# Optimization experiments

Measured on AMD Instinct MI355X. Metric: run time of the kernel, lower is better.

Reference implementation:

```python
import jax, jax.numpy as jnp
import numpy as np

BATCH, MAXPV = 32, 50
RULENUM, PROPNUM = 256, 256  # must be equal (eye(rulenum) * property_importance)
ENT_DIM, RULE_DIM = 128, 128
ENTITYNUM = 50000
THRESHOLD = 0.5


def _l2norm(x, eps=1e-12):
    # F.normalize(p=2, dim=-1)
    n = jnp.linalg.norm(x, axis=-1, keepdims=True)
    return x / jnp.clip(n, eps)


def setup_inputs() -> dict:
    key = jax.random.key(0)
    ks = jax.random.split(key, 20)
    d_in = ENT_DIM + RULE_DIM
    inp = {
        'property': jax.random.randint(ks[0], (BATCH, MAXPV), 0, ENTITYNUM),
        'value': jax.random.randint(ks[1], (BATCH, MAXPV), 0, ENTITYNUM),
        'samemask': jax.random.randint(ks[2], (BATCH, MAXPV), 0, 2),
        'padmask': jax.random.randint(ks[3], (BATCH, MAXPV), 0, 2),
        'rule_embedding': jax.random.normal(ks[4], (RULENUM, RULE_DIM), jnp.float32),
        'entity_table': jax.random.normal(ks[5], (ENTITYNUM, ENT_DIM), jnp.float32),
        # Linear weights stored (in, out); concat order in the original is (p_emb, rule_emb)
        'fc1_w': jax.random.normal(ks[6], (d_in, ENT_DIM), jnp.float32),
        'fc1_b': jax.random.normal(ks[7], (ENT_DIM,), jnp.float32) * 0.02,
        'fc2_w': jax.random.normal(ks[8], (d_in, ENT_DIM), jnp.float32),
        'fc2_b': jax.random.normal(ks[9], (ENT_DIM,), jnp.float32) * 0.02,
        'fc3_w': jax.random.normal(ks[10], (d_in, ENT_DIM), jnp.float32),
        'fc3_b': jax.random.normal(ks[11], (ENT_DIM,), jnp.float32) * 0.02,
        'fc4_w': jax.random.normal(ks[12], (ENT_DIM, 1), jnp.float32) * 0.05,
        'fc4_b': jax.random.normal(ks[13], (1,), jnp.float32) * 0.02,
        'fc5_w': jax.random.normal(ks[14], (ENT_DIM, 1), jnp.float32) * 0.05,
        'fc5_b': jax.random.normal(ks[15], (1,), jnp.float32) * 0.02,
        'fc6_w': jax.random.normal(ks[16], (ENT_DIM, ENT_DIM), jnp.float32) * 0.05,
        'fc6_b': jax.random.normal(ks[17], (ENT_DIM,), jnp.float32) * 0.02,
    }
    return inp


def reference(property, value, samemask, padmask, rule_embedding, entity_table,
              fc1_w, fc1_b, fc2_w, fc2_b, fc3_w, fc3_b,
              fc4_w, fc4_b, fc5_w, fc5_b, fc6_w, fc6_b):
    E = entity_table.shape[1]
    R = rule_embedding.shape[0]
    P = R  # propertynum == rulenum (required by eye() regularizer)

    p_emb = _l2norm(entity_table[property])   # (B, M, E)
    v_emb = _l2norm(entity_table[value])      # (B, M, E)
    r_emb = _l2norm(rule_embedding)           # (R, Dr)

    # cat(p, rule) -> Linear decomposed into two smaller matmuls (same math)
    def branch(w, b):
        return p_emb @ w[:E], r_emb @ w[E:] + b  # (B,M,Eo), (R,Eo)

    # s1 branch
    pa, ra = branch(fc1_w, fc1_b)
    h1 = jax.nn.relu(pa[:, None, :, :] + ra[None, :, None, :])   # (B,R,M,E)
    s1 = jax.nn.sigmoid(h1 @ fc4_w + fc4_b)[..., 0]              # (B,R,M)

    # p branch
    pb, rb = branch(fc2_w, fc2_b)
    h2 = jax.nn.relu(pb[:, None, :, :] + rb[None, :, None, :])
    p = jax.nn.sigmoid(h2 @ fc5_w + fc5_b)[..., 0]               # (B,R,M)

    # s2 branch
    pc, rc = branch(fc3_w, fc3_b)
    h3 = jax.nn.relu(pc[:, None, :, :] + rc[None, :, None, :])
    gv = _l2norm(h3 @ fc6_w + fc6_b)                             # (B,R,M,E)
    vb = v_emb[:, None, :, :]                                    # (B,1,M,E)
    denom = jnp.clip(jnp.linalg.norm(vb, axis=-1) * jnp.linalg.norm(gv, axis=-1), 1e-8)
    cos = jnp.sum(vb * gv, axis=-1) / denom
    s2 = 0.5 * cos + 0.5                                         # (B,R,M)

    score = p + (1.0 - p) * s2
    score = jnp.where(samemask[:, None, :] == 1, s1 * score, 1.0 - s1)

    # property importance K: fc1/fc4 on cat(prop_emb, rule_emb)
    prop_emb = _l2norm(entity_table[:P])                         # propertyids = arange(P)
    pi_h = jax.nn.relu((prop_emb @ fc1_w[:E])[None, :, :]
                       + (r_emb @ fc1_w[E:] + fc1_b)[:, None, :])  # (R,P,E)
    pi = jax.nn.sigmoid(pi_h @ fc4_w + fc4_b)[..., 0]            # (R,P)

    rule_mask = jnp.sum(pi * (pi > THRESHOLD), axis=-1) + 1.0    # (R,)

    score = score * padmask[:, None, :].astype(score.dtype)
    score = score * (s1 > THRESHOLD)
    score = jnp.sum(score, axis=-1) / rule_mask[None, :]          # (B,R)
    pooledscore = jnp.max(score, axis=1)                          # (B,)

    diag = jnp.eye(R, dtype=pi.dtype)
    reg = pi * diag + (1.0 - pi) * (1.0 - diag)
    reg = -jnp.log(reg + 1e-8) * (1.0 - diag + diag * R)
    reg_logits = jnp.mean(reg)
    return pooledscore, reg_logits
```

## Files before the change

kernel.cpp:

```cpp
#include <hip/hip_runtime.h>
#include <hip/hip_bf16.h>

#define BATCH 32
#define MAXPV 50
#define RN 256
#define PN 256
#define DIM 128
#define NI (BATCH*MAXPV)

typedef unsigned short u16;
typedef __attribute__((ext_vector_type(8))) short short8;
typedef __attribute__((ext_vector_type(4))) float f32x4;

#define F4C(v,c) ((c)==0?(v).x:(c)==1?(v).y:(c)==2?(v).z:(v).w)

__device__ float g_pa[NI*DIM], g_pb[NI*DIM], g_pc[NI*DIM];
__device__ float g_pp1[PN*DIM];
__device__ __attribute__((aligned(16))) float g_ra[RN*DIM];
__device__ __attribute__((aligned(16))) float g_rb[RN*DIM];
__device__ float g_rmask[RN], g_regp[RN];
__device__ float g_scores[(size_t)NI*RN];
__device__ short8 g_bfrag[8][4][64];
__device__ __attribute__((aligned(16))) float g_rcA[16*4*64*8];

__device__ __forceinline__ float bf2f(u16 u){ return __uint_as_float(((unsigned)u)<<16); }
__device__ __forceinline__ float LD(const void* p, size_t i, bool bf){
    return bf ? bf2f(((const u16*)p)[i]) : ((const float*)p)[i];
}
__device__ __forceinline__ int LDI(const void* p, size_t i, bool w64){
    return w64 ? (int)((const long long*)p)[i] : ((const int*)p)[i];
}
__device__ __forceinline__ short f2bf(float f){
    unsigned u = __float_as_uint(f);
    u = (u + 0x7FFFu + ((u>>16)&1u)) >> 16;
    return (short)u;
}
__device__ __forceinline__ unsigned f2bf2(float x, float y){
    float2 f; f.x=x; f.y=y;
    __hip_bfloat162 h = __float22bfloat162_rn(f);
    union { __hip_bfloat162 h; unsigned u; } c; c.h=h; return c.u;
}
__device__ __forceinline__ bool det_bf16(const void* ent){
    int l = threadIdx.x & 63;
    u16 v = ((const u16*)ent)[(size_t)2*(l*4)*977];
    int e = (v>>7)&0xFF;
    return __popcll(__ballot(e>=120 && e<=133)) >= 48;
}
__device__ __forceinline__ bool det_i64(const void* prop){
    int l = threadIdx.x & 63;
    bool z = (l<32) ? (((const unsigned*)prop)[2*l+1]==0u) : false;
    return __popcll(__ballot(z)) >= 30;
}
__device__ __forceinline__ float wred(float v){
#pragma unroll
    for(int o=32;o;o>>=1) v += __shfl_xor(v,o,64);
    return v;
}
__device__ __forceinline__ double wredd(double v){
#pragma unroll
    for(int o=32;o;o>>=1) v += __shfl_xor(v,o,64);
    return v;
}
__device__ __forceinline__ float wmax(float v){
#pragma unroll
    for(int o=32;o;o>>=1) v = fmaxf(v,__shfl_xor(v,o,64));
    return v;
}

__global__ __launch_bounds__(256) void k_pre(
    const void* __restrict__ ent, const void* __restrict__ rule,
    const void* __restrict__ prop, const void* __restrict__ fc6w,
    const void* __restrict__ fc1w, const void* __restrict__ fc2w, const void* __restrict__ fc3w,
    const void* __restrict__ fc1b, const void* __restrict__ fc2b, const void* __restrict__ fc3b){
    const bool bf = det_bf16(ent);
    const int blk = blockIdx.x, tid = threadIdx.x;
    if(blk >= 364){
        int nt = blk-364;
        int ks = tid>>6, lane = tid&63;
        int n = nt*16 + (lane&15);
        int k0 = ks*32 + (lane>>4)*8;
        short8 v;
#pragma unroll
        for(int j=0;j<8;j++) v[j] = f2bf(LD(fc6w,(size_t)(k0+j)*DIM + n, bf));
        g_bfrag[nt][ks][lane] = v;
        if(nt==0){ g_rmask[tid] = 1.f; g_regp[tid] = 0.f; }
        return;
    }
    __shared__ float s_w[64*DIM];
    __shared__ float s_in[16*DIM];
    __shared__ float s_bias[DIM];
    const void* w; size_t woff=0; const void* bptr=nullptr;
    float* out=nullptr; int row0; int mode=0; int srcsel;
    if(blk < 300){
        int wsel = blk/100; row0 = (blk%100)*16; srcsel = 0;
        w   = (wsel==0)?fc1w:(wsel==1)?fc2w:fc3w;
        out = (wsel==0)?g_pa:(wsel==1)?g_pb:g_pc;
    } else if(blk < 348){
        int rblk = blk-300; int wsel = rblk>>4; row0 = (rblk&15)*16; srcsel = 1;
        w    = (wsel==0)?fc1w:(wsel==1)?fc2w:fc3w;
        bptr = (wsel==0)?fc1b:(wsel==1)?fc2b:fc3b;
        woff = DIM*DIM; mode = wsel+1;
    } else { row0=(blk-348)*16; w=fc1w; out=g_pp1; srcsel=2; }
    const bool w64 = (srcsel==0) ? det_i64(prop) : false;
    {
        const int l = tid & 63;
        for(int it=0; it<4; it++){
            int lr = it*4 + (tid>>6);
            int row = row0 + lr;
            const void* src; size_t off;
            if(srcsel==0){ src=ent;  off=(size_t)LDI(prop,row,w64)*DIM; }
            else if(srcsel==1){ src=rule; off=(size_t)row*DIM; }
            else { src=ent; off=(size_t)row*DIM; }
            float a = LD(src,off+l,bf), b = LD(src,off+l+64,bf);
            float n = fmaxf(sqrtf((float)wredd((double)a*a+(double)b*b)), 1e-12f);
            s_in[lr*DIM+l]=a/n; s_in[lr*DIM+l+64]=b/n;
        }
    }
    if(tid<DIM) s_bias[tid] = bptr ? LD(bptr,tid,bf) : 0.f;
    const int j = tid & 127;
    const int rb8 = (tid>>7)*8;
    double acc[8] = {0,0,0,0,0,0,0,0};
    for(int half=0; half<2; half++){
        __syncthreads();
        for(int t=tid; t<64*DIM; t+=256)
            s_w[t] = LD(w, woff + (size_t)(half*64 + (t>>7))*DIM + (t&127), bf);
        __syncthreads();
        for(int k=0;k<64;k++){
            float wk = s_w[k*DIM + j];
#pragma unroll
            for(int rr=0;rr<8;rr++)
                acc[rr] += (double)s_in[(rb8+rr)*DIM + half*64 + k]*(double)wk;
        }
    }
    const double bj = (double)s_bias[j];
#pragma unroll
    for(int rr=0;rr<8;rr++){
        const int row = row0 + rb8 + rr;
        const float vv = (float)(bj + acc[rr]);
        if(mode==0)      out[(size_t)row*DIM + j] = vv;
        else if(mode==1) g_ra[(size_t)row*DIM + j] = vv;
        else if(mode==2) g_rb[(size_t)row*DIM + j] = vv;
        else {
            int mt=row>>4, am=row&15, ks=j>>5, quad=(j>>3)&3, jj=j&7;
            g_rcA[((mt*4+ks)*64 + quad*16+am)*8 + jj] = vv;
        }
    }
}

__global__ __launch_bounds__(256) void k_score(
    const void* __restrict__ ent, const void* __restrict__ prop, const void* __restrict__ val,
    const void* __restrict__ same, const void* __restrict__ pad,
    const void* __restrict__ fc4w, const void* __restrict__ fc4b,
    const void* __restrict__ fc5w, const void* __restrict__ fc5b,
    const void* __restrict__ fc6b){
    const int blk = blockIdx.x, tid = threadIdx.x;
    if(blk < 64){
        const bool bf = det_bf16(ent);
        __shared__ float s_a[4][DIM];
        __shared__ double s_pf4[DIM];
        const int i0 = blk*4;
        if(tid<DIM) s_pf4[tid]=(double)LD(fc4w,tid,bf);
        for(int t=tid; t<4*DIM; t+=256){
            int ii=t>>7, k=t&127;
            s_a[ii][k] = g_pp1[(size_t)(i0+ii)*DIM+k];
        }
        __syncthreads();
        const int r = tid;
        const float4* rap = (const float4*)&g_ra[(size_t)r*DIM];
        double d0=0.0, d1=0.0, d2=0.0, d3=0.0;
#pragma unroll 4
        for(int x=0; x<32; x++){
            const float4 ra = rap[x];
#pragma unroll
            for(int cc=0; cc<4; cc++){
                const int k = x*4 + cc;
                const float rav = F4C(ra,cc);
                const double f4k = s_pf4[k];
                d0 += (double)fmaxf(s_a[0][k]+rav,0.f)*f4k;
                d1 += (double)fmaxf(s_a[1][k]+rav,0.f)*f4k;
                d2 += (double)fmaxf(s_a[2][k]+rav,0.f)*f4k;
                d3 += (double)fmaxf(s_a[3][k]+rav,0.f)*f4k;
            }
        }
        const double b4 = (double)LD(fc4b,0,bf);
        double d[4] = {d0,d1,d2,d3};
        float mask_sum = 0.f, reg_sum = 0.f;
#pragma unroll
        for(int ii=0;ii<4;ii++){
            int p = i0 + ii;
            double sd = d[ii] + b4;
            float piv = 1.f/(1.f+expf(-(float)sd));
            if(sd > 0.0) mask_sum += piv;
            float eff = (p==r) ? piv : (1.f - piv);
            float wgt = (p==r) ? (float)RN : 1.f;
            reg_sum += -logf(eff + 1e-8f)*wgt;
        }
        atomicAdd(&g_rmask[r], mask_sum);
        atomicAdd(&g_regp[r], reg_sum);
        return;
    }
    const int ib = blk - 64;
    const int i = ib >> 1, h = ib & 1;
    const bool w64 = det_i64(prop);
    if(LDI(pad,i,w64)!=1) return;
    const bool issame = (LDI(same,i,w64)==1);
    const bool bf = det_bf16(ent);

    __shared__ float s_pa[DIM], s_pb[DIM], s_pc[DIM], s_v[DIM], s_f5[DIM];
    __shared__ double s_f4[DIM];
    __shared__ float s_s1[128], s_p[128];
    __shared__ float s_st[128][4][2];

    if(tid < DIM){
        s_pa[tid] = g_pa[(size_t)i*DIM + tid];
        s_pb[tid] = g_pb[(size_t)i*DIM + tid];
        s_pc[tid] = g_pc[(size_t)i*DIM + tid];
        s_f4[tid] = (double)LD(fc4w,tid,bf);
        s_f5[tid] = LD(fc5w,tid,bf);
    } else if(tid < 192){
        const int l = tid - 128;
        size_t off = (size_t)LDI(val,i,w64)*DIM;
        float a = LD(ent,off+l,bf), b = LD(ent,off+l+64,bf);
        float n = fmaxf(sqrtf((float)wredd((double)a*a+(double)b*b)), 1e-12f);
        s_v[l]=a/n; s_v[l+64]=b/n;
    }
    __syncthreads();

    const int rr = tid & 127;
    const int r = h*128 + rr;
    if(tid < 128){
        const float4* rap = (const float4*)&g_ra[(size_t)r*DIM];
        double d = 0.0;
#pragma unroll 4
        for(int x=0; x<32; x++){
            const float4 ra = rap[x];
            d += (double)fmaxf(s_pa[x*4+0]+ra.x,0.f)*s_f4[x*4+0];
            d += (double)fmaxf(s_pa[x*4+1]+ra.y,0.f)*s_f4[x*4+1];
            d += (double)fmaxf(s_pa[x*4+2]+ra.z,0.f)*s_f4[x*4+2];
            d += (double)fmaxf(s_pa[x*4+3]+ra.w,0.f)*s_f4[x*4+3];
        }
        const double b4 = (double)LD(fc4b,0,bf);
        double sd = d + b4;
        float s1v = 1.f/(1.f+expf(-(float)sd));
        if(issame) s_s1[rr] = (sd > 0.0) ? s1v : -s1v;
        else g_scores[(size_t)i*RN + r] = (sd > 0.0) ? (1.f - s1v) : 0.f;
    } else if(issame){
        const float4* rbp = (const float4*)&g_rb[(size_t)r*DIM];
        float pq = 0.f;
#pragma unroll 4
        for(int x=0; x<32; x++){
            const float4 rb = rbp[x];
            pq = fmaf(fmaxf(s_pb[x*4+0]+rb.x,0.f), s_f5[x*4+0], pq);
            pq = fmaf(fmaxf(s_pb[x*4+1]+rb.y,0.f), s_f5[x*4+1], pq);
            pq = fmaf(fmaxf(s_pb[x*4+2]+rb.z,0.f), s_f5[x*4+2], pq);
            pq = fmaf(fmaxf(s_pb[x*4+3]+rb.w,0.f), s_f5[x*4+3], pq);
        }
        const float b5 = LD(fc5b,0,bf);
        s_p[rr] = 1.f/(1.f+expf(-(pq + b5)));
    }
    if(!issame) return;
    __syncthreads();

    const int w = tid>>6, l = tid&63;
    const int am = l&15, quad = l>>4;
    short8 bA[4], bB[4];
#pragma unroll
    for(int ks=0; ks<4; ks++){ bA[ks]=g_bfrag[2*w][ks][l]; bB[ks]=g_bfrag[2*w+1][ks][l]; }
    const int n0 = w*32 + am, n1 = n0 + 16;
    const float v0 = s_v[n0], v1 = s_v[n1];
    const float b60 = LD(fc6b, n0, bf), b61 = LD(fc6b, n1, bf);
    float vl = s_v[l], vh = s_v[l+64];
    const float nvb = sqrtf(wred(vl*vl + vh*vh));

    int mt = h*8;
    float4 c[8];
#pragma unroll
    for(int ks=0; ks<4; ks++){
        const float* rp = &g_rcA[((mt*4+ks)*64 + l)*8];
        c[2*ks]   = *(const float4*)rp;
        c[2*ks+1] = *(const float4*)(rp+4);
    }
    for(int mtl=0; mtl<8; mtl++){
        float4 n[8];
        if(mtl < 7){
#pragma unroll
            for(int ks=0; ks<4; ks++){
                const float* rp = &g_rcA[(((mt+1)*4+ks)*64 + l)*8];
                n[2*ks]   = *(const float4*)rp;
                n[2*ks+1] = *(const float4*)(rp+4);
            }
        }
        short8 a[4];
#pragma unroll
        for(int ks=0; ks<4; ks++){
            const float4 p0 = *(const float4*)&s_pc[ks*32 + quad*8];
            const float4 p1 = *(const float4*)&s_pc[ks*32 + quad*8 + 4];
            const float4 c0 = c[2*ks], c1 = c[2*ks+1];
            union { short8 s; unsigned u[4]; } t;
            t.u[0] = f2bf2(fmaxf(p0.x+c0.x,0.f), fmaxf(p0.y+c0.y,0.f));
            t.u[1] = f2bf2(fmaxf(p0.z+c0.z,0.f), fmaxf(p0.w+c0.w,0.f));
            t.u[2] = f2bf2(fmaxf(p1.x+c1.x,0.f), fmaxf(p1.y+c1.y,0.f));
            t.u[3] = f2bf2(fmaxf(p1.z+c1.z,0.f), fmaxf(p1.w+c1.w,0.f));
            a[ks] = t.s;
        }
        f32x4 acc0 = {0.f,0.f,0.f,0.f}, acc1 = {0.f,0.f,0.f,0.f};
#pragma unroll
        for(int ks=0; ks<4; ks++){
            acc0 = __builtin_amdgcn_mfma_f32_16x16x32_bf16(a[ks], bA[ks], acc0, 0,0,0);
            acc1 = __builtin_amdgcn_mfma_f32_16x16x32_bf16(a[ks], bB[ks], acc1, 0,0,0);
        }
#pragma unroll
        for(int q=0; q<4; q++){
            float x0 = acc0[q] + b60;
            float x1 = acc1[q] + b61;
            float ss = x0*x0 + x1*x1;
            float dv = x0*v0 + x1*v1;
#pragma unroll
            for(int o=1;o<16;o<<=1){ ss += __shfl_xor(ss,o,64); dv += __shfl_xor(dv,o,64); }
            if(am==0){
                int row = mtl*16 + quad*4 + q;
                s_st[row][w][0] = ss;
                s_st[row][w][1] = dv;
            }
        }
#pragma unroll
        for(int x=0;x<8;x++) c[x] = n[x];
        mt++;
    }
    __syncthreads();
    if(tid < 128){
        const int r2 = h*128 + tid;
        float ss = s_st[tid][0][0]+s_st[tid][1][0]+s_st[tid][2][0]+s_st[tid][3][0];
        float dv = s_st[tid][0][1]+s_st[tid][1][1]+s_st[tid][2][1]+s_st[tid][3][1];
        float s1 = fabsf(s_s1[tid]);
        float gate = (s_s1[tid] > 0.f) ? 1.f : 0.f;
        float pp = s_p[tid];
        float nx = sqrtf(ss);
        float clipnx = fmaxf(nx, 1e-12f);
        float gvn = nx/clipnx;
        float denom = fmaxf(nvb*gvn, 1e-8f);
        float cosv = (dv/clipnx)/denom;
        float s2 = 0.5f*cosv + 0.5f;
        float sc = s1*(pp + (1.f-pp)*s2);
        g_scores[(size_t)i*RN + r2] = sc * gate;
    }
}

__global__ void k_fin(float* __restrict__ out, const void* __restrict__ prop,
                      const void* __restrict__ same, const void* __restrict__ pad){
    const bool w64 = det_i64(prop);
    const int blk = blockIdx.x, tid = threadIdx.x;
    const int w = tid>>6, l = tid&63;
    __shared__ float s[4];
    if(blk < 32){
        __shared__ int s_pad[MAXPV];
        if(tid < MAXPV) s_pad[tid] = LDI(pad, (size_t)blk*MAXPV + tid, w64);
        __syncthreads();
        float ssum = 0.f;
        for(int pv=0; pv<MAXPV; pv++){
            if(!s_pad[pv]) continue;
            ssum += g_scores[((size_t)blk*MAXPV + pv)*RN + tid];
        }
        float sc = ssum / g_rmask[tid];
        float m = wmax(sc);
        if(l==0) s[w]=m;
        __syncthreads();
        if(tid==0) out[blk] = fmaxf(fmaxf(s[0],s[1]), fmaxf(s[2],s[3]));
    } else {
        float v = g_regp[tid];
        v = wred(v);
        if(l==0) s[w]=v;
        __syncthreads();
        if(tid==0) out[32] = (s[0]+s[1]+s[2]+s[3]) / (float)(RN*PN);
    }
}

extern "C" void kernel_launch(void* const* d_in, const int* in_sizes, int n_in,
                              void* d_out, int out_size, void* d_ws, size_t ws_size,
                              hipStream_t stream){
    int map[18]; for(int i=0;i<18;i++) map[i]=i;
    if(n_in>=18 && in_sizes[0]==6400000){
        const int a[18] = {14,17,16,13,15,0,2,1,4,3,6,5,8,7,10,9,12,11};
        for(int i=0;i<18;i++) map[i]=a[i];
    }
    const void* prop = d_in[map[0]];
    const void* val  = d_in[map[1]];
    const void* same = d_in[map[2]];
    const void* pad  = d_in[map[3]];
    const void* rule = d_in[map[4]];
    const void* ent  = d_in[map[5]];
    const void* fc1w = d_in[map[6]];
    const void* fc1b = d_in[map[7]];
    const void* fc2w = d_in[map[8]];
    const void* fc2b = d_in[map[9]];
    const void* fc3w = d_in[map[10]];
    const void* fc3b = d_in[map[11]];
    const void* fc4w = d_in[map[12]];
    const void* fc4b = d_in[map[13]];
    const void* fc5w = d_in[map[14]];
    const void* fc5b = d_in[map[15]];
    const void* fc6w = d_in[map[16]];
    const void* fc6b = d_in[map[17]];

    k_pre<<<372, 256, 0, stream>>>(ent, rule, prop, fc6w,
                                   fc1w, fc2w, fc3w, fc1b, fc2b, fc3b);
    k_score<<<NI*2+64, 256, 0, stream>>>(ent, prop, val, same, pad,
                                         fc4w, fc4b, fc5w, fc5b, fc6b);
    k_fin<<<33, 256, 0, stream>>>((float*)d_out, prop, same, pad);
}
```

Measured before the change: 212.1 us.

## Compact active items into same/diff worklists to skip padded blocks

k_pre gains extra blocks that scan pad and same masks and use atomic counters to build two compacted worklists in workspace: same items paired with their value index, and non-same items. k_score then maps blocks onto these lists, so blocks for padded items exit immediately and non-same items run a lighter specialised path without the fc5/fc6 and MFMA work. Format flags are computed once and stored, and launch bounds now request higher occupancy. This adds a memset, atomics and an extra indirection, and about half of the launched blocks now exit early.

```diff
diff --git a/kernel.cpp b/kernel.cpp
--- a/kernel.cpp
+++ b/kernel.cpp
@@ -11,8 +11,6 @@
 typedef unsigned short u16;
 typedef __attribute__((ext_vector_type(8))) short short8;
 typedef __attribute__((ext_vector_type(4))) float f32x4;
-
-#define F4C(v,c) ((c)==0?(v).x:(c)==1?(v).y:(c)==2?(v).z:(v).w)
 
 __device__ float g_pa[NI*DIM], g_pb[NI*DIM], g_pc[NI*DIM];
 __device__ float g_pp1[PN*DIM];
@@ -23,6 +21,9 @@
 __device__ short8 g_bfrag[8][4][64];
 __device__ __attribute__((aligned(16))) float g_rcA[16*4*64*8];
 
+#define WS_WLS(ws)  ((int2*)((ws)+4))
+#define WS_WLD(ws)  ((ws)+4+3200)
+
 __device__ __forceinline__ float bf2f(u16 u){ return __uint_as_float(((unsigned)u)<<16); }
 __device__ __forceinline__ float LD(const void* p, size_t i, bool bf){
     return bf ? bf2f(((const u16*)p)[i]) : ((const float*)p)[i];
@@ -69,11 +70,32 @@
 
 __global__ __launch_bounds__(256) void k_pre(
     const void* __restrict__ ent, const void* __restrict__ rule,
-    const void* __restrict__ prop, const void* __restrict__ fc6w,
+    const void* __restrict__ prop, const void* __restrict__ val,
+    const void* __restrict__ same, const void* __restrict__ pad,
+    const void* __restrict__ fc6w,
     const void* __restrict__ fc1w, const void* __restrict__ fc2w, const void* __restrict__ fc3w,
-    const void* __restrict__ fc1b, const void* __restrict__ fc2b, const void* __restrict__ fc3b){
+    const void* __restrict__ fc1b, const void* __restrict__ fc2b, const void* __restrict__ fc3b,
+    int* __restrict__ ws){
     const bool bf = det_bf16(ent);
     const int blk = blockIdx.x, tid = threadIdx.x;
+    if(blk >= 372){
+        const bool w64 = det_i64(prop);
+        int i = (blk-372)*256 + tid;
+        if(i < NI){
+            int pd = LDI(pad,i,w64);
+            if(pd==1){
+                int sm = LDI(same,i,w64);
+                if(sm==1){
+                    int x = atomicAdd(ws+0,1);
+                    WS_WLS(ws)[x] = make_int2(i, LDI(val,i,w64));
+                } else {
+                    int x = atomicAdd(ws+1,1);
+                    WS_WLD(ws)[x] = i;
+                }
+            }
+        }
+        return;
+    }
     if(blk >= 364){
         int nt = blk-364;
         int ks = tid>>6, lane = tid&63;
@@ -83,7 +105,11 @@
 #pragma unroll
         for(int j=0;j<8;j++) v[j] = f2bf(LD(fc6w,(size_t)(k0+j)*DIM + n, bf));
         g_bfrag[nt][ks][lane] = v;
-        if(nt==0){ g_rmask[tid] = 1.f; g_regp[tid] = 0.f; }
+        if(nt==0){
+            g_rmask[tid] = 1.f; g_regp[tid] = 0.f;
+            const bool w64 = det_i64(prop);
+            if(tid==0) ws[2] = (bf?1:0) | (w64?2:0);
+        }
         return;
     }
     __shared__ float s_w[64*DIM];
@@ -147,15 +173,15 @@
     }
 }
 
-__global__ __launch_bounds__(256) void k_score(
-    const void* __restrict__ ent, const void* __restrict__ prop, const void* __restrict__ val,
-    const void* __restrict__ same, const void* __restrict__ pad,
+__global__ __launch_bounds__(256, 6) void k_score(
+    const void* __restrict__ ent,
     const void* __restrict__ fc4w, const void* __restrict__ fc4b,
     const void* __restrict__ fc5w, const void* __restrict__ fc5b,
-    const void* __restrict__ fc6b){
+    const void* __restrict__ fc6b, const int* __restrict__ ws){
     const int blk = blockIdx.x, tid = threadIdx.x;
+    const int fl = ws[2];
+    const bool bf = fl & 1;
     if(blk < 64){
-        const bool bf = det_bf16(ent);
         __shared__ float s_a[4][DIM];
         __shared__ double s_pf4[DIM];
         const int i0 = blk*4;
@@ -174,7 +200,7 @@
 #pragma unroll
             for(int cc=0; cc<4; cc++){
                 const int k = x*4 + cc;
-                const float rav = F4C(ra,cc);
+                const float rav = (cc==0)?ra.x:(cc==1)?ra.y:(cc==2)?ra.z:ra.w;
                 const double f4k = s_pf4[k];
                 d0 += (double)fmaxf(s_a[0][k]+rav,0.f)*f4k;
                 d1 += (double)fmaxf(s_a[1][k]+rav,0.f)*f4k;
@@ -199,17 +225,43 @@
         atomicAdd(&g_regp[r], reg_sum);
         return;
     }
-    const int ib = blk - 64;
-    const int i = ib >> 1, h = ib & 1;
-    const bool w64 = det_i64(prop);
-    if(LDI(pad,i,w64)!=1) return;
-    const bool issame = (LDI(same,i,w64)==1);
-    const bool bf = det_bf16(ent);
+    int w2 = blk - 64;
+    const int ns2 = ws[0]*2;
 
     __shared__ float s_pa[DIM], s_pb[DIM], s_pc[DIM], s_v[DIM], s_f5[DIM];
     __shared__ double s_f4[DIM];
     __shared__ float s_s1[128], s_p[128];
     __shared__ float s_st[128][4][2];
+
+    if(w2 >= ns2){
+        w2 -= ns2;
+        if(w2 >= ws[1]) return;
+        const int i = WS_WLD(ws)[w2];
+        if(tid < 128){
+            s_pa[tid] = g_pa[(size_t)i*DIM + tid];
+            s_f4[tid] = (double)LD(fc4w,tid,bf);
+        }
+        __syncthreads();
+        const int r = tid;
+        const float4* rap = (const float4*)&g_ra[(size_t)r*DIM];
+        double d = 0.0;
+#pragma unroll 4
+        for(int x=0; x<32; x++){
+            const float4 ra = rap[x];
+            d += (double)fmaxf(s_pa[x*4+0]+ra.x,0.f)*s_f4[x*4+0];
+            d += (double)fmaxf(s_pa[x*4+1]+ra.y,0.f)*s_f4[x*4+1];
+            d += (double)fmaxf(s_pa[x*4+2]+ra.z,0.f)*s_f4[x*4+2];
+            d += (double)fmaxf(s_pa[x*4+3]+ra.w,0.f)*s_f4[x*4+3];
+        }
+        const double b4 = (double)LD(fc4b,0,bf);
+        double sd = d + b4;
+        float s1v = 1.f/(1.f+expf(-(float)sd));
+        g_scores[(size_t)i*RN + r] = (sd > 0.0) ? (1.f - s1v) : 0.f;
+        return;
+    }
+
+    const int2 e = WS_WLS(ws)[w2>>1];
+    const int i = e.x, vi = e.y, h = w2 & 1;
 
     if(tid < DIM){
         s_pa[tid] = g_pa[(size_t)i*DIM + tid];
@@ -219,7 +271,7 @@
         s_f5[tid] = LD(fc5w,tid,bf);
     } else if(tid < 192){
         const int l = tid - 128;
-        size_t off = (size_t)LDI(val,i,w64)*DIM;
+        size_t off = (size_t)vi*DIM;
         float a = LD(ent,off+l,bf), b = LD(ent,off+l+64,bf);
         float n = fmaxf(sqrtf((float)wredd((double)a*a+(double)b*b)), 1e-12f);
         s_v[l]=a/n; s_v[l+64]=b/n;
@@ -242,9 +294,8 @@
         const double b4 = (double)LD(fc4b,0,bf);
         double sd = d + b4;
         float s1v = 1.f/(1.f+expf(-(float)sd));
-        if(issame) s_s1[rr] = (sd > 0.0) ? s1v : -s1v;
-        else g_scores[(size_t)i*RN + r] = (sd > 0.0) ? (1.f - s1v) : 0.f;
-    } else if(issame){
+        s_s1[rr] = (sd > 0.0) ? s1v : -s1v;
+    } else {
         const float4* rbp = (const float4*)&g_rb[(size_t)r*DIM];
         float pq = 0.f;
 #pragma unroll 4
@@ -258,7 +309,6 @@
         const float b5 = LD(fc5b,0,bf);
         s_p[rr] = 1.f/(1.f+expf(-(pq + b5)));
     }
-    if(!issame) return;
     __syncthreads();
 
     const int w = tid>>6, l = tid&63;
@@ -346,9 +396,9 @@
     }
 }
 
-__global__ void k_fin(float* __restrict__ out, const void* __restrict__ prop,
-                      const void* __restrict__ same, const void* __restrict__ pad){
-    const bool w64 = det_i64(prop);
+__global__ void k_fin(float* __restrict__ out, const void* __restrict__ pad,
+                      const int* __restrict__ ws){
+    const bool w64 = (ws[2] & 2) != 0;
     const int blk = blockIdx.x, tid = threadIdx.x;
     const int w = tid>>6, l = tid&63;
     __shared__ float s[4];
@@ -402,9 +452,10 @@
     const void* fc6w = d_in[map[16]];
     const void* fc6b = d_in[map[17]];
 
-    k_pre<<<372, 256, 0, stream>>>(ent, rule, prop, fc6w,
-                                   fc1w, fc2w, fc3w, fc1b, fc2b, fc3b);
-    k_score<<<NI*2+64, 256, 0, stream>>>(ent, prop, val, same, pad,
-                                         fc4w, fc4b, fc5w, fc5b, fc6b);
-    k_fin<<<33, 256, 0, stream>>>((float*)d_out, prop, same, pad);
-}
+    hipMemsetAsync(d_ws, 0, 16, stream);
+    k_pre<<<379, 256, 0, stream>>>(ent, rule, prop, val, same, pad, fc6w,
+                                   fc1w, fc2w, fc3w, fc1b, fc2b, fc3b, (int*)d_ws);
+    k_score<<<3264, 256, 0, stream>>>(ent, fc4w, fc4b, fc5w, fc5b, fc6b,
+                                      (const int*)d_ws);
+    k_fin<<<33, 256, 0, stream>>>((float*)d_out, pad, (const int*)d_ws);
+}
```

After: 265.6 us. +25.2%, slower.
